# Kernel tuning notes

Hardware: AMD Instinct MI355X
Metric: run time of the kernel (lower is better)

The kernel has to match this reference:

```python
import jax, jax.numpy as jnp
import numpy as np

N_NODES = 100000
N_EDGES = 1600000
IN_DIM = 165
HIDDEN = 128
OUT_DIM = 2


def gcn_conv(x, W, b, src, dst, n_nodes):
    """PyG GCNConv: h = x @ W; add self-loops; sym-normalized scatter-add; + bias."""
    h = x @ W  # [N, F_out]
    loop = jnp.arange(n_nodes, dtype=src.dtype)
    src_f = jnp.concatenate([src, loop])  # [E + N]
    dst_f = jnp.concatenate([dst, loop])
    deg = jax.ops.segment_sum(jnp.ones(src_f.shape[0], dtype=h.dtype), dst_f,
                              num_segments=n_nodes)  # in-degree incl. self-loop
    dinv = jnp.where(deg > 0, jax.lax.rsqrt(deg), jnp.zeros_like(deg))
    norm = dinv[src_f] * dinv[dst_f]  # [E + N]
    msg = h[src_f] * norm[:, None]  # gather + scale, [E+N, F_out]
    out = jax.ops.segment_sum(msg, dst_f, num_segments=n_nodes)  # scatter-add
    return out + b


def setup_inputs() -> dict:
    key = jax.random.key(0)
    k_x, k_e, k_w1, k_b1, k_w2, k_b2 = jax.random.split(key, 6)
    x = jax.random.normal(k_x, (N_NODES, IN_DIM), dtype=jnp.float32)
    edge_index = jax.random.randint(k_e, (2, N_EDGES), 0, N_NODES, dtype=jnp.int64)
    # Glorot-like init for linear weights, zeros for bias (PyG defaults)
    W1 = jax.random.normal(k_w1, (IN_DIM, HIDDEN), dtype=jnp.float32) / np.sqrt(IN_DIM)
    b1 = jnp.zeros((HIDDEN,), dtype=jnp.float32)
    W2 = jax.random.normal(k_w2, (HIDDEN, OUT_DIM), dtype=jnp.float32) / np.sqrt(HIDDEN)
    b2 = jnp.zeros((OUT_DIM,), dtype=jnp.float32)
    return {"x": x, "edge_index": edge_index, "W1": W1, "b1": b1, "W2": W2, "b2": b2}


def reference(x, edge_index, W1, b1, W2, b2):
    src, dst = edge_index[0], edge_index[1]
    h = gcn_conv(x, W1, b1, src, dst, N_NODES)
    h = jax.nn.relu(h)
    # dropout: eval mode (training=False) -> identity
    out = gcn_conv(h, W2, b2, src, dst, N_NODES)
    return out
```

## Files before the change

### kernel.cpp

```cpp
#include <hip/hip_runtime.h>
#include <hip/hip_fp16.h>

#define N_NODES 100000
#define N_EDGES 1600000
#define IN_DIM  165
#define HIDDEN  128
#define OUT_DIM 2

#define NBKT 196
#define CHUNK 4096
#define NCHUNK ((N_EDGES + CHUNK - 1) / CHUNK)
#define PADCAP 10240
#define KPAD 176

typedef _Float16 half8_t __attribute__((ext_vector_type(8)));
typedef _Float16 half4_t __attribute__((ext_vector_type(4)));
typedef float floatx4 __attribute__((ext_vector_type(4)));


__global__ __launch_bounds__(512) void k_part2(const int* __restrict__ src,
                                               const int* __restrict__ dst,
                                               int* __restrict__ bcnt,
                                               unsigned* __restrict__ arena) {
    __shared__ int hist[256];
    __shared__ int gbase[256];

    int t = threadIdx.x;
    int e0 = blockIdx.x * CHUNK;
    int nE = N_EDGES - e0; if (nE > CHUNK) nE = CHUNK;

    if (t < 256) hist[t] = 0;
    __syncthreads();

    for (int i = t; i < nE; i += 512)
        atomicAdd(&hist[dst[e0 + i] >> 9], 1);
    __syncthreads();

    if (t < NBKT) gbase[t] = t * PADCAP + atomicAdd(&bcnt[t], hist[t]);
    if (t < 256) hist[t] = 0;
    __syncthreads();

    for (int i = t; i < nE; i += 512) {
        int d = dst[e0 + i];
        int s = src[e0 + i];
        int bk = d >> 9;
        unsigned entry = (unsigned)s | ((unsigned)(d & 511) << 17);
        int idx = atomicAdd(&hist[bk], 1);
        arena[gbase[bk] + idx] = entry;
    }
}


__global__ __launch_bounds__(256) void k_btot(const int* __restrict__ bcnt,
                                              int* __restrict__ bucketptr) {
    __shared__ int wsum[4];
    int t = threadIdx.x, lane = t & 63, wid = t >> 6;
    int v = (t < NBKT) ? bcnt[t] : 0;
    int inc = v;
    #pragma unroll
    for (int off = 1; off < 64; off <<= 1) {
        int y = __shfl_up(inc, off);
        if (lane >= off) inc += y;
    }
    if (lane == 63) wsum[wid] = inc;
    __syncthreads();
    if (t == 0) {
        int acc = 0;
        #pragma unroll
        for (int w = 0; w < 4; w++) { int tv = wsum[w]; wsum[w] = acc; acc += tv; }
    }
    __syncthreads();
    int excl = wsum[wid] + inc - v;
    if (t <= NBKT) bucketptr[t] = (t < NBKT) ? excl : N_EDGES;
}


__global__ __launch_bounds__(1024) void k_sort3(const unsigned* __restrict__ arena,
                                                const int* __restrict__ bcnt,
                                                const int* __restrict__ bucketptr,
                                                int* __restrict__ csr,
                                                int* __restrict__ rowptr,
                                                float* __restrict__ dinv) {
    __shared__ int cnt[512];
    __shared__ int cur[512];
    __shared__ int wsum[4];
    int b = blockIdx.x;
    int n0 = b << 9;
    int t = threadIdx.x;
    int lane = t & 63, wid = t >> 6;
    int total = bcnt[b];
    int abase = b * PADCAP;
    int dbase = bucketptr[b];

    if (t < 512) cnt[t] = 0;
    __syncthreads();
    for (int p = t; p < total; p += 1024)
        atomicAdd(&cnt[arena[abase + p] >> 17], 1);
    __syncthreads();

    int c0 = 0, c1 = 0, s = 0, inc = 0;
    if (t < 256) {
        c0 = cnt[2 * t];
        c1 = cnt[2 * t + 1];
        s = c0 + c1;
        inc = s;
        #pragma unroll
        for (int off = 1; off < 64; off <<= 1) {
            int y = __shfl_up(inc, off);
            if (lane >= off) inc += y;
        }
        if (lane == 63) wsum[wid] = inc;
    }
    __syncthreads();
    if (t == 0) {
        int acc = 0;
        #pragma unroll
        for (int w = 0; w < 4; w++) { int tv = wsum[w]; wsum[w] = acc; acc += tv; }
    }
    __syncthreads();
    if (t < 256) {
        int base = dbase + wsum[wid] + (inc - s);
        cur[2 * t] = base;
        cur[2 * t + 1] = base + c0;
        int node0 = n0 + 2 * t;
        if (node0 < N_NODES) {
            rowptr[node0] = base;
            dinv[node0] = rsqrtf((float)(c0 + 1));
        }
        if (node0 + 1 < N_NODES) {
            rowptr[node0 + 1] = base + c0;
            dinv[node0 + 1] = rsqrtf((float)(c1 + 1));
        }
    }
    if (b == NBKT - 1 && t == 0) rowptr[N_NODES] = N_EDGES;
    __syncthreads();

    for (int p = t; p < total; p += 1024) {
        unsigned entry = arena[abase + p];
        int local = (int)(entry >> 17);
        int sv = (int)(entry & 0x1FFFFu);
        int pos = atomicAdd(&cur[local], 1);
        csr[pos] = sv;
    }
}


__global__ void k_w1t(const float* __restrict__ W1, _Float16* __restrict__ w1t) {
    int idx = blockIdx.x * 256 + threadIdx.x;
    if (idx < HIDDEN * KPAD) {
        int c = idx / KPAD, k = idx - c * KPAD;
        float v = (k < IN_DIM) ? W1[k * HIDDEN + c] : 0.f;
        w1t[idx] = (_Float16)v;
    }
}


__global__ __launch_bounds__(256) void k_gemm1(const float* __restrict__ x,
                                               const _Float16* __restrict__ w1t,
                                               const float* __restrict__ dinv,
                                               _Float16* __restrict__ h1s) {
    int t = threadIdx.x;
    int wid = t >> 6, lane = t & 63;
    int row0 = (blockIdx.x * 4 + wid) * 16;
    if (row0 >= N_NODES) return;
    int m = lane & 15;
    int quad = lane >> 4;
    const float* xrow = x + (size_t)(row0 + m) * IN_DIM;

    floatx4 acc[8];
    #pragma unroll
    for (int i = 0; i < 8; i++) acc[i] = (floatx4)(0.f);

    #pragma unroll
    for (int kc = 0; kc < 5; kc++) {
        int kb = kc * 32 + quad * 8;
        half8_t a;
        #pragma unroll
        for (int j = 0; j < 8; j++) a[j] = (_Float16)xrow[kb + j];
        #pragma unroll
        for (int cb = 0; cb < 8; cb++) {
            int col = cb * 16 + m;
            half8_t bf = *(const half8_t*)&w1t[col * KPAD + kb];
            acc[cb] = __builtin_amdgcn_mfma_f32_16x16x32_f16(a, bf, acc[cb], 0, 0, 0);
        }
    }
    {
        int kb = 160 + quad * 4;
        half4_t a;
        #pragma unroll
        for (int j = 0; j < 4; j++)
            a[j] = (kb + j < IN_DIM) ? (_Float16)xrow[kb + j] : (_Float16)0.f;
        #pragma unroll
        for (int cb = 0; cb < 8; cb++) {
            int col = cb * 16 + m;
            half4_t bf = *(const half4_t*)&w1t[col * KPAD + kb];
            acc[cb] = __builtin_amdgcn_mfma_f32_16x16x16f16(a, bf, acc[cb], 0, 0, 0);
        }
    }
    float dv[4];
    #pragma unroll
    for (int r = 0; r < 4; r++) dv[r] = dinv[row0 + quad * 4 + r];
    #pragma unroll
    for (int cb = 0; cb < 8; cb++) {
        #pragma unroll
        for (int r = 0; r < 4; r++) {
            h1s[(size_t)(row0 + quad * 4 + r) * HIDDEN + cb * 16 + m] =
                (_Float16)(acc[cb][r] * dv[r]);
        }
    }
}


__global__ __launch_bounds__(256) void k_agg1(const __half2* __restrict__ h1,
                                              const int* __restrict__ rowptr,
                                              const int* __restrict__ csr,
                                              const float* __restrict__ dinv,
                                              const float* __restrict__ b1,
                                              const float* __restrict__ W2,
                                              float2* __restrict__ h2s) {
    int node = blockIdx.x * 4 + (threadIdx.x >> 6);
    int f = threadIdx.x & 63;
    float2 self = __half22float2(h1[node * 64 + f]);
    float accx = self.x, accy = self.y;
    int p0 = rowptr[node], p1 = rowptr[node + 1];

    int p = p0;
    for (; p + 7 < p1; p += 8) {
        int s[8];
        #pragma unroll
        for (int j = 0; j < 8; j++) s[j] = csr[p + j];
        __half2 g[8];
        #pragma unroll
        for (int j = 0; j < 8; j++) g[j] = h1[s[j] * 64 + f];
        #pragma unroll
        for (int j = 0; j < 8; j++) {
            float2 gf = __half22float2(g[j]);
            accx += gf.x;
            accy += gf.y;
        }
    }
    for (; p < p1; p++) {
        float2 gf = __half22float2(h1[csr[p] * 64 + f]);
        accx += gf.x;
        accy += gf.y;
    }

    float di = dinv[node];
    float2 bb = ((const float2*)b1)[f];
    float z0 = fmaf(di, accx, bb.x);
    float z1 = fmaf(di, accy, bb.y);
    float r0 = fmaxf(z0, 0.f);
    float r1 = fmaxf(z1, 0.f);
    float4 w2v = ((const float4*)W2)[f];
    float a0 = r0 * w2v.x + r1 * w2v.z;
    float a1 = r0 * w2v.y + r1 * w2v.w;
    #pragma unroll
    for (int off = 32; off; off >>= 1) {
        a0 += __shfl_down(a0, off);
        a1 += __shfl_down(a1, off);
    }
    if (f == 0) h2s[node] = make_float2(di * a0, di * a1);
}


__global__ void k_agg2(const float2* __restrict__ h2s, const int* __restrict__ rowptr,
                       const int* __restrict__ csr, const float* __restrict__ dinv,
                       const float* __restrict__ b2, float2* __restrict__ out) {
    int i = blockIdx.x * blockDim.x + threadIdx.x;
    if (i >= N_NODES) return;
    float2 self = h2s[i];
    float a0 = self.x, a1 = self.y;
    int p0 = rowptr[i], p1 = rowptr[i + 1];
    int p = p0;
    for (; p + 3 < p1; p += 4) {
        int s0 = csr[p], s1 = csr[p + 1], s2 = csr[p + 2], s3 = csr[p + 3];
        float2 g0 = h2s[s0], g1 = h2s[s1], g2 = h2s[s2], g3 = h2s[s3];
        a0 += g0.x + g1.x + g2.x + g3.x;
        a1 += g0.y + g1.y + g2.y + g3.y;
    }
    for (; p < p1; p++) {
        float2 g = h2s[csr[p]];
        a0 += g.x;
        a1 += g.y;
    }
    float di = dinv[i];
    out[i] = make_float2(fmaf(di, a0, b2[0]), fmaf(di, a1, b2[1]));
}


extern "C" void kernel_launch(void* const* d_in, const int* in_sizes, int n_in,
                              void* d_out, int out_size, void* d_ws, size_t ws_size,
                              hipStream_t stream) {
    const float* x  = (const float*)d_in[0];
    const int*   ei = (const int*)d_in[1];
    const float* W1 = (const float*)d_in[2];
    const float* b1 = (const float*)d_in[3];
    const float* W2 = (const float*)d_in[4];
    const float* b2 = (const float*)d_in[5];
    float* out = (float*)d_out;

    const int* src = ei;
    const int* dst = ei + N_EDGES;

    char* ws = (char*)d_ws;
    size_t off = 0;
    auto alloc = [&](size_t bytes) -> void* {
        void* p = ws + off;
        off += (bytes + 255) & ~(size_t)255;
        return p;
    };
    _Float16* h1s    = (_Float16*)alloc((size_t)N_NODES * HIDDEN * 2);
    float*    dinv   = (float*)   alloc((size_t)N_NODES * 4);
    int*      rowptr = (int*)     alloc((size_t)(N_NODES + 1) * 4);
    int*      bcnt   = (int*)     alloc((size_t)NBKT * 4);
    int*      bktptr = (int*)     alloc((size_t)(NBKT + 1) * 4);
    unsigned* arena  = (unsigned*)alloc((size_t)NBKT * PADCAP * 4);
    int*      csr    = (int*)     alloc((size_t)N_EDGES * 4);
    _Float16* w1t    = (_Float16*)alloc((size_t)HIDDEN * KPAD * 2);
    float2*   h2s    = (float2*)  alloc((size_t)N_NODES * 8);

    (void)hipMemsetAsync(bcnt, 0, (size_t)NBKT * 4, stream);
    k_w1t<<<(HIDDEN * KPAD + 255) / 256, 256, 0, stream>>>(W1, w1t);
    k_part2<<<NCHUNK, 512, 0, stream>>>(src, dst, bcnt, arena);
    k_btot<<<1, 256, 0, stream>>>(bcnt, bktptr);
    k_sort3<<<NBKT, 1024, 0, stream>>>(arena, bcnt, bktptr, csr, rowptr, dinv);
    k_gemm1<<<(N_NODES / 16 + 3) / 4, 256, 0, stream>>>(x, w1t, dinv, h1s);
    k_agg1<<<N_NODES / 4, 256, 0, stream>>>((const __half2*)h1s, rowptr, csr, dinv, b1, W2, h2s);
    k_agg2<<<(N_NODES + 255) / 256, 256, 0, stream>>>(h2s, rowptr, csr, dinv, b2, (float2*)out);
}
```

Baseline: 266.2 us.

## Vectorize edge loads in partition/sort, x loads in GEMM, and parallelize agg2 per node

The bucket-partition and per-bucket sort kernels now read edge indices and arena entries as 128-bit int4/uint4 vectors, with scalar tails in the sort. The first GEMM loads each row of x as two four-float vectors with only 4-byte alignment assumed, since the 165-float rows are not 16-byte aligned. The second aggregation moves from one thread per node to 16 lanes per node with a shuffle reduction, which spreads the neighbour gathers across lanes for better memory-level parallelism. The aim is fewer memory instructions and less latency-bound serial gathering. The partition kernel drops its scalar tail and assumes the chunk length is a multiple of four, which holds for the fixed edge count.

```diff
diff --git a/kernel.cpp b/kernel.cpp
--- a/kernel.cpp
+++ b/kernel.cpp
@@ -16,6 +16,7 @@
 typedef _Float16 half8_t __attribute__((ext_vector_type(8)));
 typedef _Float16 half4_t __attribute__((ext_vector_type(4)));
 typedef float floatx4 __attribute__((ext_vector_type(4)));
+typedef float floatx4_a4 __attribute__((ext_vector_type(4), aligned(4)));
 
 
 __global__ __launch_bounds__(512) void k_part2(const int* __restrict__ src,
@@ -28,25 +29,38 @@
     int t = threadIdx.x;
     int e0 = blockIdx.x * CHUNK;
     int nE = N_EDGES - e0; if (nE > CHUNK) nE = CHUNK;
+    int n4 = nE >> 2;
+    const int4* dst4 = (const int4*)(dst + e0);
+    const int4* src4 = (const int4*)(src + e0);
 
     if (t < 256) hist[t] = 0;
     __syncthreads();
 
-    for (int i = t; i < nE; i += 512)
-        atomicAdd(&hist[dst[e0 + i] >> 9], 1);
+    for (int i = t; i < n4; i += 512) {
+        int4 d = dst4[i];
+        atomicAdd(&hist[d.x >> 9], 1);
+        atomicAdd(&hist[d.y >> 9], 1);
+        atomicAdd(&hist[d.z >> 9], 1);
+        atomicAdd(&hist[d.w >> 9], 1);
+    }
     __syncthreads();
 
     if (t < NBKT) gbase[t] = t * PADCAP + atomicAdd(&bcnt[t], hist[t]);
     if (t < 256) hist[t] = 0;
     __syncthreads();
 
-    for (int i = t; i < nE; i += 512) {
-        int d = dst[e0 + i];
-        int s = src[e0 + i];
-        int bk = d >> 9;
-        unsigned entry = (unsigned)s | ((unsigned)(d & 511) << 17);
-        int idx = atomicAdd(&hist[bk], 1);
-        arena[gbase[bk] + idx] = entry;
+    for (int i = t; i < n4; i += 512) {
+        int4 d = dst4[i];
+        int4 s = src4[i];
+        #pragma unroll
+        for (int j = 0; j < 4; j++) {
+            int dd = (j == 0) ? d.x : (j == 1) ? d.y : (j == 2) ? d.z : d.w;
+            int ss = (j == 0) ? s.x : (j == 1) ? s.y : (j == 2) ? s.z : s.w;
+            int bk = dd >> 9;
+            unsigned entry = (unsigned)ss | ((unsigned)(dd & 511) << 17);
+            int idx = atomicAdd(&hist[bk], 1);
+            arena[gbase[bk] + idx] = entry;
+        }
     }
 }
 
@@ -91,11 +105,22 @@
     int total = bcnt[b];
     int abase = b * PADCAP;
     int dbase = bucketptr[b];
+    int nt4 = total >> 2;
+    const uint4* arena4 = (const uint4*)(arena + abase);
 
     if (t < 512) cnt[t] = 0;
     __syncthreads();
-    for (int p = t; p < total; p += 1024)
-        atomicAdd(&cnt[arena[abase + p] >> 17], 1);
+    for (int p = t; p < nt4; p += 1024) {
+        uint4 e = arena4[p];
+        atomicAdd(&cnt[e.x >> 17], 1);
+        atomicAdd(&cnt[e.y >> 17], 1);
+        atomicAdd(&cnt[e.z >> 17], 1);
+        atomicAdd(&cnt[e.w >> 17], 1);
+    }
+    {
+        int p = (nt4 << 2) + t;
+        if (p < total) atomicAdd(&cnt[arena[abase + p] >> 17], 1);
+    }
     __syncthreads();
 
     int c0 = 0, c1 = 0, s = 0, inc = 0;
@@ -135,12 +160,26 @@
     if (b == NBKT - 1 && t == 0) rowptr[N_NODES] = N_EDGES;
     __syncthreads();
 
-    for (int p = t; p < total; p += 1024) {
-        unsigned entry = arena[abase + p];
-        int local = (int)(entry >> 17);
-        int sv = (int)(entry & 0x1FFFFu);
-        int pos = atomicAdd(&cur[local], 1);
-        csr[pos] = sv;
+    for (int p = t; p < nt4; p += 1024) {
+        uint4 e = arena4[p];
+        #pragma unroll
+        for (int j = 0; j < 4; j++) {
+            unsigned entry = (j == 0) ? e.x : (j == 1) ? e.y : (j == 2) ? e.z : e.w;
+            int local = (int)(entry >> 17);
+            int sv = (int)(entry & 0x1FFFFu);
+            int pos = atomicAdd(&cur[local], 1);
+            csr[pos] = sv;
+        }
+    }
+    {
+        int p = (nt4 << 2) + t;
+        if (p < total) {
+            unsigned entry = arena[abase + p];
+            int local = (int)(entry >> 17);
+            int sv = (int)(entry & 0x1FFFFu);
+            int pos = atomicAdd(&cur[local], 1);
+            csr[pos] = sv;
+        }
     }
 }
 
@@ -174,9 +213,13 @@
     #pragma unroll
     for (int kc = 0; kc < 5; kc++) {
         int kb = kc * 32 + quad * 8;
+        floatx4_a4 va = *(const floatx4_a4*)(xrow + kb);
+        floatx4_a4 vb = *(const floatx4_a4*)(xrow + kb + 4);
         half8_t a;
         #pragma unroll
-        for (int j = 0; j < 8; j++) a[j] = (_Float16)xrow[kb + j];
+        for (int j = 0; j < 4; j++) a[j] = (_Float16)va[j];
+        #pragma unroll
+        for (int j = 0; j < 4; j++) a[4 + j] = (_Float16)vb[j];
         #pragma unroll
         for (int cb = 0; cb < 8; cb++) {
             int col = cb * 16 + m;
@@ -263,28 +306,33 @@
 }
 
 
-__global__ void k_agg2(const float2* __restrict__ h2s, const int* __restrict__ rowptr,
-                       const int* __restrict__ csr, const float* __restrict__ dinv,
-                       const float* __restrict__ b2, float2* __restrict__ out) {
-    int i = blockIdx.x * blockDim.x + threadIdx.x;
-    if (i >= N_NODES) return;
-    float2 self = h2s[i];
-    float a0 = self.x, a1 = self.y;
-    int p0 = rowptr[i], p1 = rowptr[i + 1];
-    int p = p0;
-    for (; p + 3 < p1; p += 4) {
-        int s0 = csr[p], s1 = csr[p + 1], s2 = csr[p + 2], s3 = csr[p + 3];
-        float2 g0 = h2s[s0], g1 = h2s[s1], g2 = h2s[s2], g3 = h2s[s3];
-        a0 += g0.x + g1.x + g2.x + g3.x;
-        a1 += g0.y + g1.y + g2.y + g3.y;
-    }
-    for (; p < p1; p++) {
+__global__ __launch_bounds__(256) void k_agg2(const float2* __restrict__ h2s,
+                                              const int* __restrict__ rowptr,
+                                              const int* __restrict__ csr,
+                                              const float* __restrict__ dinv,
+                                              const float* __restrict__ b2,
+                                              float2* __restrict__ out) {
+    int wid = threadIdx.x >> 6, lane = threadIdx.x & 63;
+    int sub = lane >> 4, el = lane & 15;
+    int node = blockIdx.x * 16 + wid * 4 + sub;
+    int p0 = rowptr[node], p1 = rowptr[node + 1];
+    float ax = 0.f, ay = 0.f;
+    for (int p = p0 + el; p < p1; p += 16) {
         float2 g = h2s[csr[p]];
-        a0 += g.x;
-        a1 += g.y;
-    }
-    float di = dinv[i];
-    out[i] = make_float2(fmaf(di, a0, b2[0]), fmaf(di, a1, b2[1]));
+        ax += g.x;
+        ay += g.y;
+    }
+    #pragma unroll
+    for (int off = 8; off; off >>= 1) {
+        ax += __shfl_xor(ax, off);
+        ay += __shfl_xor(ay, off);
+    }
+    if (el == 0) {
+        float2 self = h2s[node];
+        float di = dinv[node];
+        out[node] = make_float2(fmaf(di, self.x + ax, b2[0]),
+                                fmaf(di, self.y + ay, b2[1]));
+    }
 }
 
 
@@ -326,5 +374,5 @@
     k_sort3<<<NBKT, 1024, 0, stream>>>(arena, bcnt, bktptr, csr, rowptr, dinv);
     k_gemm1<<<(N_NODES / 16 + 3) / 4, 256, 0, stream>>>(x, w1t, dinv, h1s);
     k_agg1<<<N_NODES / 4, 256, 0, stream>>>((const __half2*)h1s, rowptr, csr, dinv, b1, W2, h2s);
-    k_agg2<<<(N_NODES + 255) / 256, 256, 0, stream>>>(h2s, rowptr, csr, dinv, b2, (float2*)out);
-}
+    k_agg2<<<N_NODES / 16, 256, 0, stream>>>(h2s, rowptr, csr, dinv, b2, (float2*)out);
+}
```

After: 260.6 us. 1.02x faster.
